# Optimization experiments

Hardware: AMD Instinct MI355X
Metric: run time of the kernel (lower is better)

Reference implementation:

```python
import jax, jax.numpy as jnp
import numpy as np

N_VTS = 4
NUM_HEADS = 12

def setup_inputs() -> dict:
    key = jax.random.key(0)
    ks = jax.random.split(key, 7)
    B_, N, C = 1024, 68, 768
    x = jax.random.normal(ks[0], (B_, N, C), dtype=jnp.float32)
    pe = jax.random.normal(ks[1], (128, C), dtype=jnp.float32)
    mask = jnp.zeros((B_, N, N), dtype=jnp.float32)
    # learned params: qkv Linear(C, 3C, bias), proj Linear(C, C, bias)
    s = 1.0 / np.sqrt(C)
    w_qkv = jax.random.normal(ks[2], (3 * C, C), dtype=jnp.float32) * s
    b_qkv = jnp.zeros((3 * C,), dtype=jnp.float32)
    w_proj = jax.random.normal(ks[3], (C, C), dtype=jnp.float32) * s
    b_proj = jnp.zeros((C,), dtype=jnp.float32)
    return {"x": x, "pe": pe, "mask": mask, "w_qkv": w_qkv, "b_qkv": b_qkv,
            "w_proj": w_proj, "b_proj": b_proj}

def reference(x, pe, mask, w_qkv, b_qkv, w_proj, b_proj):
    B_, N, C = x.shape
    H = NUM_HEADS
    hd = C // H
    scale = hd ** (-0.5)
    # center-crop pe to the N - n_vts non-virtual tokens and add
    N_ = N - N_VTS
    m = pe.shape[0]
    strt = m // 2 - N_ // 2
    x = x.at[:, N_VTS:, :].add(pe[strt:strt + N_])
    # qkv projection -> (3, B_, H, N, hd)
    qkv = (x @ w_qkv.T + b_qkv).reshape(B_, N, 3, H, hd).transpose(2, 0, 3, 1, 4)
    q, k, v = qkv[0] * scale, qkv[1], qkv[2]
    attn = jnp.einsum('bhnd,bhmd->bhnm', q, k) + mask[:, None, :, :]
    attn = jax.nn.softmax(attn, axis=-1)
    out = jnp.einsum('bhnm,bhmd->bhnd', attn, v)
    out = out.transpose(0, 2, 1, 3).reshape(B_, N, C)
    return out @ w_proj.T + b_proj
```

## Files before the change

### kernel.cpp

```cpp
#include <hip/hip_runtime.h>
#include <hip/hip_bf16.h>
#include <stdint.h>

static constexpr int BATCH = 1024;
static constexpr int NTOK  = 68;
static constexpr int CDIM  = 768;
static constexpr int NHEAD = 12;
static constexpr int M_ROWS = BATCH * NTOK;
static constexpr int KDIM   = CDIM;

typedef float  f32x4  __attribute__((ext_vector_type(4)));
typedef __bf16 bf16x8 __attribute__((ext_vector_type(8)));

__device__ __forceinline__ f32x4 mfma16(bf16x8 a, bf16x8 b, f32x4 c) {
  return __builtin_amdgcn_mfma_f32_16x16x32_bf16(a, b, c, 0, 0, 0);
}

__device__ __forceinline__ void async_ld16(void* lds, const void* g) {
  __builtin_amdgcn_global_load_lds((const __attribute__((address_space(1))) void*)g,
                                   (__attribute__((address_space(3))) void*)lds,
                                   16, 0, 0);
}

__device__ __forceinline__ void store4bf16(__hip_bfloat16* dst, f32x4 v) {
  __hip_bfloat16 tmp[4];
  tmp[0] = __float2bfloat16(v[0]);
  tmp[1] = __float2bfloat16(v[1]);
  tmp[2] = __float2bfloat16(v[2]);
  tmp[3] = __float2bfloat16(v[3]);
  *(uint2*)dst = *(const uint2*)tmp;
}

__global__ __launch_bounds__(256) void cvt_bf16(const float* __restrict__ src,
                                                __hip_bfloat16* __restrict__ dst, int n4) {
  int i = blockIdx.x * 256 + threadIdx.x;
  if (i >= n4) return;
  f32x4 v = ((const f32x4*)src)[i];
  store4bf16(dst + (size_t)i * 4, v);
}

__global__ __launch_bounds__(256) void prep_x(const float* __restrict__ x,
                                              const float* __restrict__ pe,
                                              __hip_bfloat16* __restrict__ xb) {
  int i = blockIdx.x * 256 + threadIdx.x;
  int m  = i / 192;
  int c4 = i - m * 192;
  int n  = m % 68;
  f32x4 v = ((const f32x4*)x)[i];
  if (n >= 4) {
    f32x4 p = ((const f32x4*)pe)[(n + 28) * 192 + c4];
    v[0] += p[0]; v[1] += p[1]; v[2] += p[2]; v[3] += p[3];
  }
  store4bf16(xb + (size_t)i * 4, v);
}

template<int EPI>
__global__ __launch_bounds__(256)
void gemm_bt(const __hip_bfloat16* __restrict__ A,
             const __hip_bfloat16* __restrict__ Bm,
             const float* __restrict__ bias,
             __hip_bfloat16* __restrict__ qo,
             __hip_bfloat16* __restrict__ ko,
             __hip_bfloat16* __restrict__ vo,
             float* __restrict__ out,
             int K) {
  __shared__ __align__(16) char lds[32768];
  char* lA = lds;
  char* lB = lds + 16384;

  const int tid  = threadIdx.x;
  const int w    = tid >> 6;
  const int lane = tid & 63;
  const int m0 = blockIdx.y * 128;
  const int n0 = blockIdx.x * 128;
  const int lrow = lane >> 3, slot = lane & 7;
  const size_t ldb = (size_t)K * 2;

  f32x4 acc[4][4];
#pragma unroll
  for (int i = 0; i < 4; ++i)
#pragma unroll
    for (int j = 0; j < 4; ++j) acc[i][j] = (f32x4){0.f, 0.f, 0.f, 0.f};

  const int wr = w >> 1, wc = w & 1;
  const int fr = lane & 15, fkb = (lane >> 4) << 4;

  const char* Ab = (const char*)A;
  const char* Bb = (const char*)Bm;

  for (int kt = 0; kt < K; kt += 64) {
#pragma unroll
    for (int c2 = 0; c2 < 4; ++c2) {
      int rb = c2 * 32 + w * 8;
      int r  = rb + lrow;
      int sk = (slot ^ (r & 7)) << 4;
      async_ld16(lA + rb * 128, Ab + (size_t)(m0 + r) * ldb + (size_t)kt * 2 + sk);
      async_ld16(lB + rb * 128, Bb + (size_t)(n0 + r) * ldb + (size_t)kt * 2 + sk);
    }
    __syncthreads();
#pragma unroll
    for (int k0 = 0; k0 < 2; ++k0) {
      bf16x8 af[4], bfv[4];
#pragma unroll
      for (int i = 0; i < 4; ++i) {
        int ra = wr * 64 + i * 16 + fr;
        af[i] = *(const bf16x8*)(lA + ra * 128 + ((k0 * 64 + fkb) ^ ((ra & 7) << 4)));
        int rbB = wc * 64 + i * 16 + fr;
        bfv[i] = *(const bf16x8*)(lB + rbB * 128 + ((k0 * 64 + fkb) ^ ((rbB & 7) << 4)));
      }
#pragma unroll
      for (int i = 0; i < 4; ++i)
#pragma unroll
        for (int j = 0; j < 4; ++j)
          acc[i][j] = mfma16(af[i], bfv[j], acc[i][j]);
    }
    __syncthreads();
  }

#pragma unroll
  for (int i = 0; i < 4; ++i) {
#pragma unroll
    for (int j = 0; j < 4; ++j) {
#pragma unroll
      for (int r = 0; r < 4; ++r) {
        int m  = m0 + wr * 64 + i * 16 + ((lane >> 4) << 2) + r;
        int jj = n0 + wc * 64 + j * 16 + (lane & 15);
        float val = acc[i][j][r] + bias[jj];
        if (EPI == 0) {
          int which = (jj >= 1536) ? 2 : (jj >= 768 ? 1 : 0);
          int jl = jj - which * 768;
          int h = jl >> 6, d = jl & 63;
          if (which == 0) val *= 0.125f;
          int bb = m / 68, n = m - bb * 68;
          __hip_bfloat16* dst = (which == 0) ? qo : (which == 1 ? ko : vo);
          dst[((size_t)(bb * 12 + h) * 68 + n) * 64 + d] = __float2bfloat16(val);
        } else {
          out[(size_t)m * 768 + jj] = val;
        }
      }
    }
  }
}

__global__ __launch_bounds__(256)
void attn(const __hip_bfloat16* __restrict__ q,
          const __hip_bfloat16* __restrict__ kk,
          const __hip_bfloat16* __restrict__ vv,
          const float* __restrict__ mask,
          __hip_bfloat16* __restrict__ ao) {
  __shared__ __align__(16) char sm[63808];
  char*  Pq = sm;
  char*  Kl = sm + 15360;
  char*  Vt = sm + 25600;
  float* S  = (float*)(sm + 37888);

  const int tid  = threadIdx.x;
  const int w    = tid >> 6;
  const int lane = tid & 63;
  const int bh = blockIdx.x, b = bh / 12, h = bh - b * 12;

  for (int e = tid; e < 15952; e += 256) ((uint32_t*)sm)[e] = 0u;
  __syncthreads();

  const __hip_bfloat16* qg = q  + (size_t)bh * 4352;
  const __hip_bfloat16* kg = kk + (size_t)bh * 4352;
  const __hip_bfloat16* vg = vv + (size_t)bh * 4352;

  for (int e = tid; e < 544; e += 256) {
    int row = e >> 3, slot = e & 7;
    int off = row * 128 + (((slot << 4)) ^ ((row & 7) << 4));
    *(bf16x8*)(Pq + off) = *(const bf16x8*)(qg + e * 8);
    *(bf16x8*)(Kl + off) = *(const bf16x8*)(kg + e * 8);
  }
  for (int e = tid; e < 544; e += 256) {
    int j = e >> 3, d8 = e & 7;
    bf16x8 vx = *(const bf16x8*)(vg + e * 8);
#pragma unroll
    for (int u = 0; u < 8; ++u) {
      int d = d8 * 8 + u;
      *(__bf16*)(Vt + d * 192 + ((2 * j) ^ ((d & 3) << 4))) = vx[u];
    }
  }
  __syncthreads();

  const int fr = lane & 15, fkb = (lane >> 4) << 4;

  for (int t = w; t < 25; t += 4) {
    int ti = t / 5, tj = t - ti * 5;
    f32x4 a4 = (f32x4){0.f, 0.f, 0.f, 0.f};
#pragma unroll
    for (int k0 = 0; k0 < 2; ++k0) {
      int ra = ti * 16 + fr;
      bf16x8 af = *(const bf16x8*)(Pq + ra * 128 + ((k0 * 64 + fkb) ^ ((ra & 7) << 4)));
      int rb = tj * 16 + fr;
      bf16x8 bf_ = *(const bf16x8*)(Kl + rb * 128 + ((k0 * 64 + fkb) ^ ((rb & 7) << 4)));
      a4 = mfma16(af, bf_, a4);
    }
#pragma unroll
    for (int r = 0; r < 4; ++r)
      S[(ti * 16 + ((lane >> 4) << 2) + r) * 81 + tj * 16 + (lane & 15)] = a4[r];
  }
  __syncthreads();

  const float* mb = mask + (size_t)b * 4624;
  for (int e = tid; e < 4624; e += 256) {
    int i = e / 68, j = e - i * 68;
    S[i * 81 + j] += mb[e];
  }
  __syncthreads();

  if (tid < 68) {
    float mx = -1e30f;
    for (int j = 0; j < 68; ++j) mx = fmaxf(mx, S[tid * 81 + j]);
    float sum = 0.f;
    for (int j = 0; j < 68; ++j) {
      float p = __expf(S[tid * 81 + j] - mx);
      S[tid * 81 + j] = p;
      sum += p;
    }
    float inv = 1.0f / sum;
    int swz = (tid & 3) << 4;
    for (int j = 0; j < 68; ++j)
      *(__bf16*)(Pq + tid * 192 + ((2 * j) ^ swz)) = (__bf16)(S[tid * 81 + j] * inv);
    for (int j = 68; j < 96; ++j)
      *(__bf16*)(Pq + tid * 192 + ((2 * j) ^ swz)) = (__bf16)0.f;
  }
  __syncthreads();

  for (int t = w; t < 20; t += 4) {
    int ti = t >> 2, td = t & 3;
    f32x4 a4 = (f32x4){0.f, 0.f, 0.f, 0.f};
#pragma unroll
    for (int k0 = 0; k0 < 3; ++k0) {
      int ra = ti * 16 + fr;
      bf16x8 af = *(const bf16x8*)(Pq + ra * 192 + ((k0 * 64 + fkb) ^ ((ra & 3) << 4)));
      int rb = td * 16 + fr;
      bf16x8 bf_ = *(const bf16x8*)(Vt + rb * 192 + ((k0 * 64 + fkb) ^ ((rb & 3) << 4)));
      a4 = mfma16(af, bf_, a4);
    }
#pragma unroll
    for (int r = 0; r < 4; ++r) {
      int i = ti * 16 + ((lane >> 4) << 2) + r;
      if (i < 68)
        ao[((size_t)(b * 68 + i)) * 768 + h * 64 + td * 16 + (lane & 15)] =
            __float2bfloat16(a4[r]);
    }
  }
}

extern "C" void kernel_launch(void* const* d_in, const int* in_sizes, int n_in,
                              void* d_out, int out_size, void* d_ws, size_t ws_size,
                              hipStream_t stream) {
  const float* x     = (const float*)d_in[0];
  const float* pe    = (const float*)d_in[1];
  const float* mask  = (const float*)d_in[2];
  const float* wqkv  = (const float*)d_in[3];
  const float* bqkv  = (const float*)d_in[4];
  const float* wproj = (const float*)d_in[5];
  const float* bproj = (const float*)d_in[6];
  float* out = (float*)d_out;

  char* ws = (char*)d_ws;
  const size_t SZ = 106954752;
  __hip_bfloat16* xb  = (__hip_bfloat16*)(ws);
  __hip_bfloat16* qb  = (__hip_bfloat16*)(ws + SZ);
  __hip_bfloat16* kb  = (__hip_bfloat16*)(ws + 2 * SZ);
  __hip_bfloat16* vb  = (__hip_bfloat16*)(ws + 3 * SZ);
  __hip_bfloat16* wqb = (__hip_bfloat16*)(ws + 4 * SZ);
  __hip_bfloat16* wpb = (__hip_bfloat16*)(ws + 4 * SZ + 3538944);

  cvt_bf16<<<1728, 256, 0, stream>>>(wqkv, wqb, 442368);
  cvt_bf16<<<576, 256, 0, stream>>>(wproj, wpb, 147456);
  prep_x<<<52224, 256, 0, stream>>>(x, pe, xb);
  gemm_bt<0><<<dim3(18, 544), 256, 0, stream>>>(xb, wqb, bqkv, qb, kb, vb, nullptr, KDIM);
  attn<<<12288, 256, 0, stream>>>(qb, kb, vb, mask, xb);
  gemm_bt<1><<<dim3(6, 544), 256, 0, stream>>>(xb, wpb, bproj, nullptr, nullptr, nullptr, out, KDIM);
}
```

Measured before the change: 1.336 ms.

## Swizzle block order for XCD locality, hoist epilogue math, vectorize softmax

```diff
diff --git a/kernel.cpp b/kernel.cpp
--- a/kernel.cpp
+++ b/kernel.cpp
@@ -2,12 +2,7 @@
 #include <hip/hip_bf16.h>
 #include <stdint.h>
 
-static constexpr int BATCH = 1024;
-static constexpr int NTOK  = 68;
-static constexpr int CDIM  = 768;
-static constexpr int NHEAD = 12;
-static constexpr int M_ROWS = BATCH * NTOK;
-static constexpr int KDIM   = CDIM;
+static constexpr int KDIM = 768;
 
 typedef float  f32x4  __attribute__((ext_vector_type(4)));
 typedef __bf16 bf16x8 __attribute__((ext_vector_type(8)));
@@ -63,7 +58,7 @@
              __hip_bfloat16* __restrict__ ko,
              __hip_bfloat16* __restrict__ vo,
              float* __restrict__ out,
-             int K) {
+             int K, int nbx) {
   __shared__ __align__(16) char lds[32768];
   char* lA = lds;
   char* lB = lds + 16384;
@@ -71,8 +66,14 @@
   const int tid  = threadIdx.x;
   const int w    = tid >> 6;
   const int lane = tid & 63;
-  const int m0 = blockIdx.y * 128;
-  const int n0 = blockIdx.x * 128;
+
+  const int id  = blockIdx.x;
+  const int swz = (id & 7) * ((int)gridDim.x >> 3) + (id >> 3);
+  const int by  = swz / nbx;
+  const int bx  = swz - by * nbx;
+  const int m0 = by * 128;
+  const int n0 = bx * 128;
+
   const int lrow = lane >> 3, slot = lane & 7;
   const size_t ldb = (size_t)K * 2;
 
@@ -117,26 +118,36 @@
     __syncthreads();
   }
 
+  float bj[4];
+  int hj[4], dj[4];
+  const int which = (EPI == 0) ? (n0 >= 1536 ? 2 : (n0 >= 768 ? 1 : 0)) : 0;
+#pragma unroll
+  for (int j = 0; j < 4; ++j) {
+    int jc = wc * 64 + j * 16 + (lane & 15);
+    bj[j] = bias[n0 + jc];
+    int jl = (n0 - which * 768) + jc;
+    hj[j] = jl >> 6;
+    dj[j] = jl & 63;
+  }
+  __hip_bfloat16* dst = (EPI == 0) ? (which == 0 ? qo : (which == 1 ? ko : vo)) : nullptr;
+  const float scl = (EPI == 0 && which == 0) ? 0.125f : 1.0f;
+
 #pragma unroll
   for (int i = 0; i < 4; ++i) {
 #pragma unroll
-    for (int j = 0; j < 4; ++j) {
-#pragma unroll
-      for (int r = 0; r < 4; ++r) {
-        int m  = m0 + wr * 64 + i * 16 + ((lane >> 4) << 2) + r;
-        int jj = n0 + wc * 64 + j * 16 + (lane & 15);
-        float val = acc[i][j][r] + bias[jj];
-        if (EPI == 0) {
-          int which = (jj >= 1536) ? 2 : (jj >= 768 ? 1 : 0);
-          int jl = jj - which * 768;
-          int h = jl >> 6, d = jl & 63;
-          if (which == 0) val *= 0.125f;
-          int bb = m / 68, n = m - bb * 68;
-          __hip_bfloat16* dst = (which == 0) ? qo : (which == 1 ? ko : vo);
-          dst[((size_t)(bb * 12 + h) * 68 + n) * 64 + d] = __float2bfloat16(val);
-        } else {
-          out[(size_t)m * 768 + jj] = val;
-        }
+    for (int r = 0; r < 4; ++r) {
+      int m = m0 + wr * 64 + i * 16 + ((lane >> 4) << 2) + r;
+      if (EPI == 0) {
+        int bb = m / 68, n = m - bb * 68;
+        size_t base = (size_t)bb * 12 * 4352 + (size_t)n * 64;
+#pragma unroll
+        for (int j = 0; j < 4; ++j)
+          dst[base + (size_t)hj[j] * 4352 + dj[j]] =
+              __float2bfloat16((acc[i][j][r] + bj[j]) * scl);
+      } else {
+#pragma unroll
+        for (int j = 0; j < 4; ++j)
+          out[(size_t)m * 768 + n0 + wc * 64 + j * 16 + (lane & 15)] = acc[i][j][r] + bj[j];
       }
     }
   }
@@ -148,19 +159,19 @@
           const __hip_bfloat16* __restrict__ vv,
           const float* __restrict__ mask,
           __hip_bfloat16* __restrict__ ao) {
-  __shared__ __align__(16) char sm[63808];
+  __shared__ __align__(16) char sm[65088];
   char*  Pq = sm;
   char*  Kl = sm + 15360;
   char*  Vt = sm + 25600;
   float* S  = (float*)(sm + 37888);
+  float* Si = (float*)(sm + 64768);
 
   const int tid  = threadIdx.x;
   const int w    = tid >> 6;
   const int lane = tid & 63;
-  const int bh = blockIdx.x, b = bh / 12, h = bh - b * 12;
-
-  for (int e = tid; e < 15952; e += 256) ((uint32_t*)sm)[e] = 0u;
-  __syncthreads();
+  const int bid = blockIdx.x;
+  const int bh  = (bid & 7) * 1536 + (bid >> 3);
+  const int b = bh / 12, h = bh - b * 12;
 
   const __hip_bfloat16* qg = q  + (size_t)bh * 4352;
   const __hip_bfloat16* kg = kk + (size_t)bh * 4352;
@@ -168,7 +179,7 @@
 
   for (int e = tid; e < 544; e += 256) {
     int row = e >> 3, slot = e & 7;
-    int off = row * 128 + (((slot << 4)) ^ ((row & 7) << 4));
+    int off = row * 128 + ((slot << 4) ^ ((row & 7) << 4));
     *(bf16x8*)(Pq + off) = *(const bf16x8*)(qg + e * 8);
     *(bf16x8*)(Kl + off) = *(const bf16x8*)(kg + e * 8);
   }
@@ -180,6 +191,10 @@
       int d = d8 * 8 + u;
       *(__bf16*)(Vt + d * 192 + ((2 * j) ^ ((d & 3) << 4))) = vx[u];
     }
+  }
+  for (int e = tid; e < 1792; e += 256) {
+    int d = e / 28, j = 68 + e - d * 28;
+    *(__bf16*)(Vt + d * 192 + ((2 * j) ^ ((d & 3) << 4))) = (__bf16)0.f;
   }
   __syncthreads();
 
@@ -198,32 +213,56 @@
     }
 #pragma unroll
     for (int r = 0; r < 4; ++r)
-      S[(ti * 16 + ((lane >> 4) << 2) + r) * 81 + tj * 16 + (lane & 15)] = a4[r];
+      S[(ti * 16 + ((lane >> 4) << 2) + r) * 84 + tj * 16 + (lane & 15)] = a4[r];
   }
   __syncthreads();
 
   const float* mb = mask + (size_t)b * 4624;
   for (int e = tid; e < 4624; e += 256) {
     int i = e / 68, j = e - i * 68;
-    S[i * 81 + j] += mb[e];
+    S[i * 84 + j] += mb[e];
   }
   __syncthreads();
 
   if (tid < 68) {
-    float mx = -1e30f;
-    for (int j = 0; j < 68; ++j) mx = fmaxf(mx, S[tid * 81 + j]);
+    const f32x4* Srow = (const f32x4*)(S + tid * 84);
+    f32x4 m4 = Srow[0];
+#pragma unroll
+    for (int i = 1; i < 17; ++i) {
+      f32x4 v = Srow[i];
+      m4[0] = fmaxf(m4[0], v[0]); m4[1] = fmaxf(m4[1], v[1]);
+      m4[2] = fmaxf(m4[2], v[2]); m4[3] = fmaxf(m4[3], v[3]);
+    }
+    float mx = fmaxf(fmaxf(m4[0], m4[1]), fmaxf(m4[2], m4[3]));
     float sum = 0.f;
-    for (int j = 0; j < 68; ++j) {
-      float p = __expf(S[tid * 81 + j] - mx);
-      S[tid * 81 + j] = p;
-      sum += p;
-    }
-    float inv = 1.0f / sum;
-    int swz = (tid & 3) << 4;
-    for (int j = 0; j < 68; ++j)
-      *(__bf16*)(Pq + tid * 192 + ((2 * j) ^ swz)) = (__bf16)(S[tid * 81 + j] * inv);
-    for (int j = 68; j < 96; ++j)
-      *(__bf16*)(Pq + tid * 192 + ((2 * j) ^ swz)) = (__bf16)0.f;
+    char* Prow = Pq + tid * 192;
+    const int swzb = (tid & 3) << 4;
+#pragma unroll
+    for (int ib = 0; ib < 12; ++ib) {
+      bf16x8 pk;
+      if (ib < 8) {
+        f32x4 a = Srow[2 * ib], c = Srow[2 * ib + 1];
+#pragma unroll
+        for (int u = 0; u < 4; ++u) {
+          float pa = __expf(a[u] - mx), pc = __expf(c[u] - mx);
+          sum += pa + pc;
+          pk[u] = (__bf16)pa; pk[4 + u] = (__bf16)pc;
+        }
+      } else if (ib == 8) {
+        f32x4 a = Srow[16];
+#pragma unroll
+        for (int u = 0; u < 4; ++u) {
+          float pa = __expf(a[u] - mx);
+          sum += pa;
+          pk[u] = (__bf16)pa; pk[4 + u] = (__bf16)0.f;
+        }
+      } else {
+#pragma unroll
+        for (int u = 0; u < 8; ++u) pk[u] = (__bf16)0.f;
+      }
+      *(bf16x8*)(Prow + ((ib * 16) ^ swzb)) = pk;
+    }
+    Si[tid] = 1.0f / sum;
   }
   __syncthreads();
 
@@ -241,9 +280,11 @@
 #pragma unroll
     for (int r = 0; r < 4; ++r) {
       int i = ti * 16 + ((lane >> 4) << 2) + r;
-      if (i < 68)
+      if (i < 68) {
+        float inv = Si[i];
         ao[((size_t)(b * 68 + i)) * 768 + h * 64 + td * 16 + (lane & 15)] =
-            __float2bfloat16(a4[r]);
+            __float2bfloat16(a4[r] * inv);
+      }
     }
   }
 }
@@ -272,7 +313,7 @@
   cvt_bf16<<<1728, 256, 0, stream>>>(wqkv, wqb, 442368);
   cvt_bf16<<<576, 256, 0, stream>>>(wproj, wpb, 147456);
   prep_x<<<52224, 256, 0, stream>>>(x, pe, xb);
-  gemm_bt<0><<<dim3(18, 544), 256, 0, stream>>>(xb, wqb, bqkv, qb, kb, vb, nullptr, KDIM);
+  gemm_bt<0><<<9792, 256, 0, stream>>>(xb, wqb, bqkv, qb, kb, vb, nullptr, KDIM, 18);
   attn<<<12288, 256, 0, stream>>>(qb, kb, vb, mask, xb);
-  gemm_bt<1><<<dim3(6, 544), 256, 0, stream>>>(xb, wpb, bproj, nullptr, nullptr, nullptr, out, KDIM);
-}
+  gemm_bt<1><<<3264, 256, 0, stream>>>(xb, wpb, bproj, nullptr, nullptr, nullptr, out, KDIM, 6);
+}
```

Result: faster. 1.153 ms (-13.7%).
